# Kernel optimization log

Hardware: AMD Instinct MI355X
Metric: run time of the kernel (lower is better)

Reference implementation:

```python
import jax, jax.numpy as jnp
import numpy as np

B, T, E, D, N, L, NF = 4, 2048, 512, 512, 16, 4, 2048


def setup_inputs() -> dict:
    key = jax.random.key(0)
    ks = jax.random.split(key, 12)
    r = lambda k, s, sc=1.0: jax.random.normal(k, s, dtype=jnp.float32) * sc
    return {
        "text_emb": r(ks[0], (B, T, E)),
        "W_in": r(ks[1], (E, D), 1.0 / np.sqrt(E).astype(np.float32)),
        "b_in": jnp.zeros((D,), jnp.float32),
        "freq_pe": r(ks[2], (NF, D), 0.02),
        # diagonal-SSM (S4D) params per layer, stacked on leading L axis
        "A_log": r(ks[3], (L, D, N), 0.5),
        "B_ssm": r(ks[4], (L, D, N), 0.5),
        "C_ssm": r(ks[5], (L, D, N), 0.5),
        "log_dt": r(ks[6], (L, D), 0.5) - 4.6,  # dt ~ 0.01
        "D_skip": r(ks[7], (L, D), 0.5),
        "ln_f0_scale": jnp.ones((D,), jnp.float32),
        "ln_f0_bias": jnp.zeros((D,), jnp.float32),
        "W_f0": r(ks[8], (D, 1), 1.0 / np.sqrt(D).astype(np.float32)),
        "b_f0": jnp.zeros((1,), jnp.float32),
        "ln_en_scale": jnp.ones((D,), jnp.float32),
        "ln_en_bias": jnp.zeros((D,), jnp.float32),
        "W_en": r(ks[9], (D, 1), 1.0 / np.sqrt(D).astype(np.float32)),
        "b_en": jnp.zeros((1,), jnp.float32),
    }


def _layernorm(x, scale, bias, eps=1e-5):
    mu = jnp.mean(x, axis=-1, keepdims=True)
    var = jnp.mean(jnp.square(x - mu), axis=-1, keepdims=True)
    return (x - mu) * jax.lax.rsqrt(var + eps) * scale + bias


def _s4_layer(h, A_log, Bm, Cm, log_dt, Dsk):
    # h: [B, T, D]; diagonal SSM with ZOH discretization, scanned over T.
    dt = jnp.exp(log_dt)                 # [D]
    A = -jnp.exp(A_log)                  # [D, N], stable (negative real)
    Abar = jnp.exp(dt[:, None] * A)      # [D, N]
    Bbar = (Abar - 1.0) / A * Bm         # [D, N]
    u_t = jnp.transpose(h, (1, 0, 2))    # [T, B, D]
    x0 = jnp.zeros((h.shape[0], h.shape[2], A.shape[1]), h.dtype)  # [B, D, N]

    def step(x, u):
        x = Abar * x + Bbar * u[..., None]          # [B, D, N]
        y = jnp.einsum('bdn,dn->bd', x, Cm)         # readout
        return x, y

    _, ys = jax.lax.scan(step, x0, u_t)             # ys: [T, B, D]
    y = jnp.transpose(ys, (1, 0, 2)) + Dsk * h      # D skip connection
    return h + jax.nn.gelu(y)                       # residual + activation


def _forward(text_emb, W_in, b_in, freq_pe, A_log, B_ssm, C_ssm, log_dt,
             D_skip, ln_f0_scale, ln_f0_bias, W_f0, b_f0,
             ln_en_scale, ln_en_bias, W_en, b_en):
    x = text_emb @ W_in + b_in                      # [B, T, D]
    Tlen = x.shape[1]
    nf = freq_pe.shape[0]
    if nf >= Tlen:                                  # static-shape crop
        freq = freq_pe[:Tlen]
    else:                                           # static-shape edge pad
        pad = jnp.repeat(freq_pe[-1:], Tlen - nf, axis=0)
        freq = jnp.concatenate([freq_pe, pad], axis=0)
    h = x + freq[None, :, :]
    for l in range(A_log.shape[0]):
        h = _s4_layer(h, A_log[l], B_ssm[l], C_ssm[l], log_dt[l], D_skip[l])
    f0 = (_layernorm(h, ln_f0_scale, ln_f0_bias) @ W_f0 + b_f0)[..., 0]
    en = (_layernorm(h, ln_en_scale, ln_en_bias) @ W_en + b_en)[..., 0]
    return f0, en


def reference(text_emb, W_in, b_in, freq_pe, A_log, B_ssm, C_ssm, log_dt,
              D_skip, ln_f0_scale, ln_f0_bias, W_f0, b_f0,
              ln_en_scale, ln_en_bias, W_en, b_en):
    return _forward(text_emb, W_in, b_in, freq_pe, A_log, B_ssm, C_ssm,
                    log_dt, D_skip, ln_f0_scale, ln_f0_bias, W_f0, b_f0,
                    ln_en_scale, ln_en_bias, W_en, b_en)
```

## Files before the change

### kernel.cpp

```cpp
#include <hip/hip_runtime.h>

#define B_   4
#define T_   2048
#define E_   512
#define D_   512
#define N_   16
#define L_   4
#define TCH  16
#define US_  65

typedef __bf16 bf16x8 __attribute__((ext_vector_type(8)));
typedef float  f32x4  __attribute__((ext_vector_type(4)));
typedef float  f32x2  __attribute__((ext_vector_type(2)));
typedef unsigned short us8 __attribute__((ext_vector_type(8)));

__device__ __forceinline__ float us2f(unsigned short u) {
    return __uint_as_float(((unsigned int)u) << 16);
}
__device__ __forceinline__ unsigned short f2us(float f) {
    unsigned int u = __float_as_uint(f);
    unsigned int r = (u + 0x7fffu + ((u >> 16) & 1u)) >> 16;
    return (unsigned short)r;
}
__device__ __forceinline__ float ldin(const void* p, int i, unsigned int f) {
    return f ? ((const float*)p)[i] : us2f(((const unsigned short*)p)[i]);
}
__device__ __forceinline__ unsigned int probe_f32(const void* lnfs) {
    return (((const unsigned int*)lnfs)[0] == 0x3F800000u) ? 1u : 0u;
}
__device__ __forceinline__ f32x2 pk_fma(f32x2 a, f32x2 b, f32x2 c) {
    f32x2 d;
    asm("v_pk_fma_f32 %0, %1, %2, %3" : "=v"(d) : "v"(a), "v"(b), "v"(c));
    return d;
}
__device__ __forceinline__ f32x2 pk_mul(f32x2 a, f32x2 b) {
    f32x2 d;
    asm("v_pk_mul_f32 %0, %1, %2" : "=v"(d) : "v"(a), "v"(b));
    return d;
}
template<int CTRL, int RM>
__device__ __forceinline__ f32x2 dpp2(f32x2 v) {
    f32x2 r;
    r[0] = __int_as_float(__builtin_amdgcn_update_dpp(0, __float_as_int(v[0]), CTRL, RM, 0xF, true));
    r[1] = __int_as_float(__builtin_amdgcn_update_dpp(0, __float_as_int(v[1]), CTRL, RM, 0xF, true));
    return r;
}

#define PA    0
#define PB    32768
#define PC    65536
#define PDT   98304
#define PDSK  100352
#define PLFS  102400
#define PLFB  102912
#define PWF   103424
#define PLES  103936
#define PLEB  104448
#define PWEN  104960
#define PSC   105472
#define PRM_N 105474

#define NB_TEXT 2048
#define NB_PRM  413
#define NB_WT   64
#define NB_S4P  128

__global__ __launch_bounds__(256) void prep_kernel(
    const void* X, const void* Win,
    const void* A_log, const void* B_ssm, const void* C_ssm,
    const void* log_dt, const void* D_skip,
    const void* lnfs, const void* lnfb, const void* Wf0,
    const void* lnes, const void* lneb, const void* Wen,
    const void* bf0, const void* ben,
    unsigned short* __restrict__ textc, unsigned short* __restrict__ Wt,
    float* __restrict__ P, float* __restrict__ P2) {
    __shared__ float tile[64 * 65];
    unsigned int f = probe_f32(lnfs);
    int bid = blockIdx.x;
    if (bid < NB_TEXT) {
        int i = (bid * 256 + threadIdx.x) * 8;
        if (f) {
            const float* xf = (const float*)X;
            us8 r;
#pragma unroll
            for (int j = 0; j < 8; j++) r[j] = f2us(xf[i + j]);
            *(us8*)(textc + i) = r;
        } else {
            *(us8*)(textc + i) = *(const us8*)((const unsigned short*)X + i);
        }
    } else if (bid < NB_TEXT + NB_PRM) {
        int i = (bid - NB_TEXT) * 256 + threadIdx.x;
        if      (i < PB)     P[i] = ldin(A_log,  i - PA,   f);
        else if (i < PC)     P[i] = ldin(B_ssm,  i - PB,   f);
        else if (i < PDT)    P[i] = ldin(C_ssm,  i - PC,   f);
        else if (i < PDSK)   P[i] = ldin(log_dt, i - PDT,  f);
        else if (i < PLFS)   P[i] = ldin(D_skip, i - PDSK, f);
        else if (i < PLFB)   P[i] = ldin(lnfs,   i - PLFS, f);
        else if (i < PWF)    P[i] = ldin(lnfb,   i - PLFB, f);
        else if (i < PLES)   P[i] = ldin(Wf0,    i - PWF,  f);
        else if (i < PLEB)   P[i] = ldin(lnes,   i - PLES, f);
        else if (i < PWEN)   P[i] = ldin(lneb,   i - PLEB, f);
        else if (i < PSC)    P[i] = ldin(Wen,    i - PWEN, f);
        else if (i == PSC)     P[i] = ldin(bf0, 0, f);
        else if (i == PSC + 1) P[i] = ldin(ben, 0, f);
    } else if (bid < NB_TEXT + NB_PRM + NB_WT) {
        int tb = bid - (NB_TEXT + NB_PRM);
        int d0 = (tb >> 3) * 64, e0 = (tb & 7) * 64;
        int r = threadIdx.x >> 6, i = threadIdx.x & 63;
#pragma unroll
        for (int k = 0; k < 16; k++) {
            int e = k * 4 + r;
            tile[e * 65 + i] = ldin(Win, (e0 + e) * D_ + d0 + i, f);
        }
        __syncthreads();
#pragma unroll
        for (int k = 0; k < 16; k++) {
            int dd = k * 4 + r;
            Wt[(size_t)(d0 + dd) * E_ + e0 + i] = f2us(tile[i * 65 + dd]);
        }
    } else {
        int i = (bid - (NB_TEXT + NB_PRM + NB_WT)) * 256 + threadIdx.x;
        int n = i & 15;
        int ld = i >> 4;
        float dt = __expf(ldin(log_dt, ld, f));
        float A  = -__expf(ldin(A_log, i, f));
        float Ab = __expf(dt * A);
        float Bb = (Ab - 1.f) / A * ldin(B_ssm, i, f);
        float l2M = 23.083120654223414f * dt * A;
        int base = ld * 64 + n;
        P2[base]      = Ab;
        P2[base + 16] = Bb * ldin(C_ssm, i, f);
        P2[base + 32] = exp2f(l2M);
        P2[base + 48] = l2M;
    }
}

__global__ __launch_bounds__(256) void gemm_kernel(const unsigned short* __restrict__ X,
                                                   const unsigned short* __restrict__ Wt,
                                                   const void* __restrict__ freq,
                                                   const void* __restrict__ b_in,
                                                   const void* __restrict__ lnfs,
                                                   float* __restrict__ H) {
    __shared__ unsigned short wlds[64 * 264];
    const unsigned int fl = probe_f32(lnfs);
    const int tid = threadIdx.x;
    const int w  = tid >> 6;
    const int ln = tid & 15;
    const int q  = (tid >> 4) & 3;
    const int d0 = blockIdx.x * 64;
    const int t0 = blockIdx.y * 128;
    const int b  = blockIdx.z;

    f32x4 acc[2][4];
#pragma unroll
    for (int i = 0; i < 2; i++)
#pragma unroll
        for (int j = 0; j < 4; j++) { acc[i][j][0]=0.f; acc[i][j][1]=0.f; acc[i][j][2]=0.f; acc[i][j][3]=0.f; }

    const size_t xbase = ((size_t)b * T_ + t0) * E_;

#pragma unroll
    for (int p = 0; p < 2; ++p) {
        if (p) __syncthreads();
#pragma unroll
        for (int it = 0; it < 8; ++it) {
            int flat = it * 256 + tid;
            int d = flat >> 5;
            int e = (flat & 31) << 3;
            bf16x8 v = *(const bf16x8*)(Wt + (size_t)(d0 + d) * E_ + p * 256 + e);
            *(bf16x8*)(wlds + d * 264 + e) = v;
        }
        __syncthreads();
#pragma unroll
        for (int s = 0; s < 8; ++s) {
            const int eo = s * 32 + q * 8;
            bf16x8 bfr[4];
#pragma unroll
            for (int j = 0; j < 4; j++)
                bfr[j] = *(const bf16x8*)(wlds + (j * 16 + ln) * 264 + eo);
#pragma unroll
            for (int sub = 0; sub < 2; ++sub) {
                const int t = w * 32 + sub * 16 + ln;
                bf16x8 afr = *(const bf16x8*)(X + xbase + (size_t)t * E_ + p * 256 + eo);
#pragma unroll
                for (int j = 0; j < 4; j++)
                    acc[sub][j] = __builtin_amdgcn_mfma_f32_16x16x32_bf16(afr, bfr[j], acc[sub][j], 0, 0, 0);
            }
        }
    }
#pragma unroll
    for (int sub = 0; sub < 2; ++sub) {
#pragma unroll
        for (int j = 0; j < 4; j++) {
            int d  = d0 + j * 16 + ln;
            int tb = t0 + w * 32 + sub * 16 + q * 4;
            float bi = ldin(b_in, d, fl);
            f32x4 o;
#pragma unroll
            for (int r4 = 0; r4 < 4; r4++)
                o[r4] = acc[sub][j][r4] + ldin(freq, (tb + r4) * D_ + d, fl) + bi;
            *(f32x4*)(H + ((size_t)b * D_ + d) * T_ + tb) = o;
        }
    }
}

__global__ __launch_bounds__(256) __attribute__((amdgpu_waves_per_eu(4, 4)))
void s4_kernel(float* __restrict__ H, const float* __restrict__ P,
               const float* __restrict__ P2) {
    __shared__ float xl[4][TCH * US_];
    __shared__ float hstate[2][2][16];
    const int w = threadIdx.x >> 6, lane = threadIdx.x & 63;
    const int rp = w >> 1, half = w & 1;
    const int row = blockIdx.x * 2 + rp;
    const int d = row & (D_ - 1);
    float* Xw  = xl[w];
    float* Xme = Xw + lane;
    float* gp  = H + (size_t)row * T_ + half * 1024;

#pragma unroll
    for (int k = 0; k < 4; k++) {
        int m = k * 256 + lane * 4;
        f32x4 v = *(const f32x4*)(gp + m);
#pragma unroll
        for (int i = 0; i < 4; i++) {
            int t = m + i;
            Xw[(t & 15) * US_ + (t >> 4)] = v[i];
        }
    }

    for (int l = 0; l < L_; ++l) {
        const float* pp = P2 + (size_t)(((l << 9) + d) << 6);
        float Dsk = P[PDSK + l * D_ + d];
        f32x2 Ab[8], CB[8];
#pragma unroll
        for (int n = 0; n < 8; n++) {
            Ab[n] = *(const f32x2*)(pp + 2 * n);
            CB[n] = *(const f32x2*)(pp + 16 + 2 * n);
        }
        f32x2 b[8];
#pragma unroll
        for (int n = 0; n < 8; n++) { b[n][0] = 0.f; b[n][1] = 0.f; }
#pragma unroll 8
        for (int j = 0; j < TCH; j++) {
            float uu = Xme[j * US_];
            f32x2 u2; u2[0] = uu; u2[1] = uu;
#pragma unroll
            for (int n = 0; n < 8; n++) b[n] = pk_fma(Ab[n], b[n], u2);
        }
        {
            f32x2 M1[8], w1[8], w2[8];
            float e1  = (float)((lane & 15) + 1);
            float e2l = (float)((lane & 31) + 1);
#pragma unroll
            for (int n = 0; n < 8; n++) {
                M1[n] = *(const f32x2*)(pp + 32 + 2 * n);
                f32x2 l2m = *(const f32x2*)(pp + 48 + 2 * n);
                w1[n][0] = exp2f(l2m[0] * e1);  w1[n][1] = exp2f(l2m[1] * e1);
                w2[n][0] = exp2f(l2m[0] * e2l); w2[n][1] = exp2f(l2m[1] * e2l);
            }
#pragma unroll
            for (int n = 0; n < 8; n++) b[n] = pk_fma(M1[n], dpp2<0x111, 0xF>(b[n]), b[n]);
#pragma unroll
            for (int n = 0; n < 8; n++) M1[n] = pk_mul(M1[n], M1[n]);
#pragma unroll
            for (int n = 0; n < 8; n++) b[n] = pk_fma(M1[n], dpp2<0x112, 0xF>(b[n]), b[n]);
#pragma unroll
            for (int n = 0; n < 8; n++) M1[n] = pk_mul(M1[n], M1[n]);
#pragma unroll
            for (int n = 0; n < 8; n++) b[n] = pk_fma(M1[n], dpp2<0x114, 0xF>(b[n]), b[n]);
#pragma unroll
            for (int n = 0; n < 8; n++) M1[n] = pk_mul(M1[n], M1[n]);
#pragma unroll
            for (int n = 0; n < 8; n++) b[n] = pk_fma(M1[n], dpp2<0x118, 0xF>(b[n]), b[n]);
#pragma unroll
            for (int n = 0; n < 8; n++) b[n] = pk_fma(w1[n], dpp2<0x142, 0xA>(b[n]), b[n]);
#pragma unroll
            for (int n = 0; n < 8; n++) b[n] = pk_fma(w2[n], dpp2<0x143, 0xC>(b[n]), b[n]);
        }
        if (half == 0 && lane == 63) {
#pragma unroll
            for (int n = 0; n < 8; n++) {
                hstate[rp][l & 1][2 * n]     = b[n][0];
                hstate[rp][l & 1][2 * n + 1] = b[n][1];
            }
        }
        f32x2 z[8];
#pragma unroll
        for (int n = 0; n < 8; n++) {
            z[n][0] = __shfl_up(b[n][0], 1u, 64);
            z[n][1] = __shfl_up(b[n][1], 1u, 64);
            if (lane == 0) { z[n][0] = 0.f; z[n][1] = 0.f; }
        }
        __syncthreads();
        if (half) {
            float el = (float)lane;
            const float* hs = hstate[rp][l & 1];
#pragma unroll
            for (int n = 0; n < 8; n++) {
                f32x2 l2m = *(const f32x2*)(pp + 48 + 2 * n);
                f32x2 wh; wh[0] = exp2f(l2m[0] * el); wh[1] = exp2f(l2m[1] * el);
                f32x2 h0; h0[0] = hs[2 * n]; h0[1] = hs[2 * n + 1];
                z[n] = pk_fma(wh, h0, z[n]);
            }
        }
#pragma unroll 8
        for (int j = 0; j < TCH; j++) {
            float uu = Xme[j * US_];
            f32x2 u2; u2[0] = uu; u2[1] = uu;
#pragma unroll
            for (int n = 0; n < 8; n++) z[n] = pk_fma(Ab[n], z[n], u2);
            f32x2 ya; ya[0] = 0.f; ya[1] = 0.f;
            f32x2 yb; yb[0] = 0.f; yb[1] = 0.f;
#pragma unroll
            for (int n = 0; n < 8; n += 2) {
                ya = pk_fma(CB[n], z[n], ya);
                yb = pk_fma(CB[n + 1], z[n + 1], yb);
            }
            f32x2 s = ya + yb;
            float y = fmaf(Dsk, uu, s[0] + s[1]);
            float zin = 0.7978845608028654f * fmaf(0.044715f, y * y * y, y);
            float e2  = __expf(2.f * zin);
            float r   = __builtin_amdgcn_rcpf(e2 + 1.f);
            Xme[j * US_] = (uu + y) - y * r;
        }
    }
#pragma unroll
    for (int k = 0; k < 4; k++) {
        int m = k * 256 + lane * 4;
        f32x4 v;
#pragma unroll
        for (int i = 0; i < 4; i++) {
            int t = m + i;
            v[i] = Xw[(t & 15) * US_ + (t >> 4)];
        }
        *(f32x4*)(gp + m) = v;
    }
}

__global__ __launch_bounds__(256) void final_kernel(const float* __restrict__ H,
                                                    const float* __restrict__ P,
                                                    void* __restrict__ out,
                                                    const void* __restrict__ lnfs_raw) {
    __shared__ float red[4][8][64];
    unsigned int f = probe_f32(lnfs_raw);
    int tid = threadIdx.x;
    int w = tid >> 6, tl = tid & 63;
    int tg = blockIdx.x * 64 + tl;
    int b = tg >> 11, t = tg & (T_ - 1);
    float S1=0.f,S2=0.f,Pf=0.f,Pe=0.f,Cf=0.f,Ce=0.f,Df=0.f,De=0.f;
    const float* hp = H + ((size_t)b * D_) * T_ + t;
#pragma unroll 4
    for (int i = 0; i < 128; i++) {
        int d = w * 128 + i;
        float hv = hp[(size_t)d * T_];
        float sf = P[PLFS + d], bfv = P[PLFB + d], wf = P[PWF + d];
        float se = P[PLES + d], bev = P[PLEB + d], we = P[PWEN + d];
        S1 += hv; S2 = fmaf(hv, hv, S2);
        float tf = sf * wf, te = se * we;
        Pf = fmaf(hv, tf, Pf); Pe = fmaf(hv, te, Pe);
        Cf += tf; Ce += te;
        Df = fmaf(bfv, wf, Df); De = fmaf(bev, we, De);
    }
    red[w][0][tl]=S1; red[w][1][tl]=S2; red[w][2][tl]=Pf; red[w][3][tl]=Pe;
    red[w][4][tl]=Cf; red[w][5][tl]=Ce; red[w][6][tl]=Df; red[w][7][tl]=De;
    __syncthreads();
    if (w == 0) {
        float a[8];
#pragma unroll
        for (int k = 0; k < 8; k++)
            a[k] = red[0][k][tl] + red[1][k][tl] + red[2][k][tl] + red[3][k][tl];
        float mu  = a[0] * (1.f / 512.f);
        float var = a[1] * (1.f / 512.f) - mu * mu;
        float r   = rsqrtf(var + 1e-5f);
        float f0  = r * (a[2] - mu * a[4]) + a[6] + P[PSC + 0];
        float en  = r * (a[3] - mu * a[5]) + a[7] + P[PSC + 1];
        if (f) {
            ((float*)out)[tg]           = f0;
            ((float*)out)[B_ * T_ + tg] = en;
        } else {
            ((unsigned short*)out)[tg]           = f2us(f0);
            ((unsigned short*)out)[B_ * T_ + tg] = f2us(en);
        }
    }
}

extern "C" void kernel_launch(void* const* d_in, const int* in_sizes, int n_in,
                              void* d_out, int out_size, void* d_ws, size_t ws_size,
                              hipStream_t stream) {
    (void)in_sizes; (void)n_in; (void)out_size; (void)ws_size;
    float* ws = (float*)d_ws;
    float* P     = ws;
    float* H     = ws + 105504;
    unsigned short* textc = (unsigned short*)(ws + 4299808);
    unsigned short* Wt    = (unsigned short*)(ws + 6396960);
    float* P2    = ws + 6528032;

    prep_kernel<<<dim3(NB_TEXT + NB_PRM + NB_WT + NB_S4P), dim3(256), 0, stream>>>(
        d_in[0], d_in[1], d_in[4], d_in[5], d_in[6], d_in[7], d_in[8],
        d_in[9], d_in[10], d_in[11], d_in[13], d_in[14], d_in[15],
        d_in[12], d_in[16], textc, Wt, P, P2);
    gemm_kernel<<<dim3(8, 16, 4), dim3(256), 0, stream>>>(textc, Wt, d_in[3], d_in[2], d_in[9], H);
    s4_kernel<<<dim3(1024), dim3(256), 0, stream>>>(H, P, P2);
    final_kernel<<<dim3(128), dim3(256), 0, stream>>>(H, P, d_out, d_in[9]);
}
```

Baseline: 177.4 us.

## Keep per-lane sequence chunk in registers instead of LDS transpose buffer

Each lane now loads its contiguous 16-element time chunk straight from global memory into a register array and keeps it there across all four layers. This removes the shared-memory transpose buffer and the LDS reads and writes in both scan loops. The w2 weights are now built from w1 and the squared M1 factor instead of a second set of exp2f calls. The C and D-skip parameter loads are moved to just before the output loop to shorten their live range. The cost is higher register pressure and uncoalesced per-lane 64-byte global accesses, in exchange for no LDS traffic.

Result: no change. 174.8 us (-1.4%).

```diff
diff --git a/kernel.cpp b/kernel.cpp
--- a/kernel.cpp
+++ b/kernel.cpp
@@ -7,7 +7,6 @@
 #define N_   16
 #define L_   4
 #define TCH  16
-#define US_  65
 
 typedef __bf16 bf16x8 __attribute__((ext_vector_type(8)));
 typedef float  f32x4  __attribute__((ext_vector_type(4)));
@@ -207,56 +206,43 @@
 __global__ __launch_bounds__(256) __attribute__((amdgpu_waves_per_eu(4, 4)))
 void s4_kernel(float* __restrict__ H, const float* __restrict__ P,
                const float* __restrict__ P2) {
-    __shared__ float xl[4][TCH * US_];
     __shared__ float hstate[2][2][16];
     const int w = threadIdx.x >> 6, lane = threadIdx.x & 63;
     const int rp = w >> 1, half = w & 1;
     const int row = blockIdx.x * 2 + rp;
     const int d = row & (D_ - 1);
-    float* Xw  = xl[w];
-    float* Xme = Xw + lane;
-    float* gp  = H + (size_t)row * T_ + half * 1024;
-
+    float* gp = H + (size_t)row * T_ + half * 1024 + lane * TCH;
+
+    float u[TCH];
 #pragma unroll
     for (int k = 0; k < 4; k++) {
-        int m = k * 256 + lane * 4;
-        f32x4 v = *(const f32x4*)(gp + m);
-#pragma unroll
-        for (int i = 0; i < 4; i++) {
-            int t = m + i;
-            Xw[(t & 15) * US_ + (t >> 4)] = v[i];
-        }
+        f32x4 v = *(const f32x4*)(gp + k * 4);
+        u[k * 4] = v[0]; u[k * 4 + 1] = v[1]; u[k * 4 + 2] = v[2]; u[k * 4 + 3] = v[3];
     }
 
     for (int l = 0; l < L_; ++l) {
         const float* pp = P2 + (size_t)(((l << 9) + d) << 6);
-        float Dsk = P[PDSK + l * D_ + d];
-        f32x2 Ab[8], CB[8];
-#pragma unroll
-        for (int n = 0; n < 8; n++) {
-            Ab[n] = *(const f32x2*)(pp + 2 * n);
-            CB[n] = *(const f32x2*)(pp + 16 + 2 * n);
-        }
+        f32x2 Ab[8];
+#pragma unroll
+        for (int n = 0; n < 8; n++) Ab[n] = *(const f32x2*)(pp + 2 * n);
         f32x2 b[8];
 #pragma unroll
         for (int n = 0; n < 8; n++) { b[n][0] = 0.f; b[n][1] = 0.f; }
-#pragma unroll 8
+#pragma unroll
         for (int j = 0; j < TCH; j++) {
-            float uu = Xme[j * US_];
-            f32x2 u2; u2[0] = uu; u2[1] = uu;
+            f32x2 u2; u2[0] = u[j]; u2[1] = u[j];
 #pragma unroll
             for (int n = 0; n < 8; n++) b[n] = pk_fma(Ab[n], b[n], u2);
         }
         {
             f32x2 M1[8], w1[8], w2[8];
-            float e1  = (float)((lane & 15) + 1);
-            float e2l = (float)((lane & 31) + 1);
+            float e1 = (float)((lane & 15) + 1);
+            bool hi16 = (lane & 16) != 0;
 #pragma unroll
             for (int n = 0; n < 8; n++) {
                 M1[n] = *(const f32x2*)(pp + 32 + 2 * n);
                 f32x2 l2m = *(const f32x2*)(pp + 48 + 2 * n);
                 w1[n][0] = exp2f(l2m[0] * e1);  w1[n][1] = exp2f(l2m[1] * e1);
-                w2[n][0] = exp2f(l2m[0] * e2l); w2[n][1] = exp2f(l2m[1] * e2l);
             }
 #pragma unroll
             for (int n = 0; n < 8; n++) b[n] = pk_fma(M1[n], dpp2<0x111, 0xF>(b[n]), b[n]);
@@ -272,6 +258,13 @@
             for (int n = 0; n < 8; n++) M1[n] = pk_mul(M1[n], M1[n]);
 #pragma unroll
             for (int n = 0; n < 8; n++) b[n] = pk_fma(M1[n], dpp2<0x118, 0xF>(b[n]), b[n]);
+#pragma unroll
+            for (int n = 0; n < 8; n++) {
+                f32x2 M16 = pk_mul(M1[n], M1[n]);
+                f32x2 wm  = pk_mul(w1[n], M16);
+                w2[n][0] = hi16 ? wm[0] : w1[n][0];
+                w2[n][1] = hi16 ? wm[1] : w1[n][1];
+            }
 #pragma unroll
             for (int n = 0; n < 8; n++) b[n] = pk_fma(w1[n], dpp2<0x142, 0xA>(b[n]), b[n]);
 #pragma unroll
@@ -303,9 +296,13 @@
                 z[n] = pk_fma(wh, h0, z[n]);
             }
         }
-#pragma unroll 8
+        float Dsk = P[PDSK + l * D_ + d];
+        f32x2 CB[8];
+#pragma unroll
+        for (int n = 0; n < 8; n++) CB[n] = *(const f32x2*)(pp + 16 + 2 * n);
+#pragma unroll
         for (int j = 0; j < TCH; j++) {
-            float uu = Xme[j * US_];
+            float uu = u[j];
             f32x2 u2; u2[0] = uu; u2[1] = uu;
 #pragma unroll
             for (int n = 0; n < 8; n++) z[n] = pk_fma(Ab[n], z[n], u2);
@@ -321,19 +318,14 @@
             float zin = 0.7978845608028654f * fmaf(0.044715f, y * y * y, y);
             float e2  = __expf(2.f * zin);
             float r   = __builtin_amdgcn_rcpf(e2 + 1.f);
-            Xme[j * US_] = (uu + y) - y * r;
+            u[j] = (uu + y) - y * r;
         }
     }
 #pragma unroll
     for (int k = 0; k < 4; k++) {
-        int m = k * 256 + lane * 4;
         f32x4 v;
-#pragma unroll
-        for (int i = 0; i < 4; i++) {
-            int t = m + i;
-            v[i] = Xw[(t & 15) * US_ + (t >> 4)];
-        }
-        *(f32x4*)(gp + m) = v;
+        v[0] = u[k * 4]; v[1] = u[k * 4 + 1]; v[2] = u[k * 4 + 2]; v[3] = u[k * 4 + 3];
+        *(f32x4*)(gp + k * 4) = v;
     }
 }
 
```
